# Optimization experiments

Measured on AMD Instinct MI355X. Metric: run time of the kernel, lower is better.

Reference implementation:

```python
import jax, jax.numpy as jnp
import numpy as np

V, E, H, B, T = 50000, 300, 512, 256, 64
D_OUT = 3
EPS = 1e-5


def setup_inputs() -> dict:
    key = jax.random.key(0)
    ks = jax.random.split(key, 16)
    s = lambda k, shape: (jax.random.normal(k, shape, jnp.float32) * 0.05)
    return {
        "premise": jax.random.randint(ks[0], (T, B), 0, V),
        "hypothesis": jax.random.randint(ks[1], (T, B), 0, V),
        "embed": s(ks[2], (V, E)),
        "W_ih": s(ks[3], (4 * H, E)),
        "W_hh": s(ks[4], (4 * H, H)),
        "b_ih": s(ks[5], (4 * H,)),
        "b_hh": s(ks[6], (4 * H,)),
        "bn0_g": jnp.ones((4 * H,), jnp.float32),
        "bn0_b": jnp.zeros((4 * H,), jnp.float32),
        "W0": s(ks[7], (4 * H, 4 * H)),
        "b0": s(ks[8], (4 * H,)),
        "bn1_g": jnp.ones((4 * H,), jnp.float32),
        "bn1_b": jnp.zeros((4 * H,), jnp.float32),
        "W1": s(ks[9], (4 * H, 4 * H)),
        "b1": s(ks[10], (4 * H,)),
        "bno_g": jnp.ones((4 * H,), jnp.float32),
        "bno_b": jnp.zeros((4 * H,), jnp.float32),
        "Wo": s(ks[11], (D_OUT, 4 * H)),
        "bo": s(ks[12], (D_OUT,)),
    }


def _lstm_final_h(xs, W_ih, W_hh, bias):
    # xs: [T, N, E]; shared-weight LSTMCell scan, returns final hidden [N, H]
    x_proj = jnp.einsum('tne,ge->tng', xs, W_ih) + bias  # hoist input GEMM out of the recurrence
    n = xs.shape[1]
    h0 = jnp.zeros((n, H), xs.dtype)

    def step(carry, xg):
        h, c = carry
        gates = xg + h @ W_hh.T
        i, f, g, o = jnp.split(gates, 4, axis=-1)  # torch LSTMCell gate order
        c = jax.nn.sigmoid(f) * c + jax.nn.sigmoid(i) * jnp.tanh(g)
        h = jax.nn.sigmoid(o) * jnp.tanh(c)
        return (h, c), None

    (h, _), _ = jax.lax.scan(step, (h0, h0), x_proj)
    return h


def _bn(x, g, b):
    # BatchNorm1d in training mode: biased batch stats
    mu = x.mean(0)
    var = x.var(0)
    return (x - mu) * jax.lax.rsqrt(var + EPS) * g + b


def reference(premise, hypothesis, embed, W_ih, W_hh, b_ih, b_hh,
              bn0_g, bn0_b, W0, b0, bn1_g, bn1_b, W1, b1,
              bno_g, bno_b, Wo, bo):
    p = embed[premise]      # [T, B, E]
    hyp = embed[hypothesis]  # [T, B, E]
    combined = jnp.concatenate([p, hyp], axis=1)  # [T, 2B, E]
    bias = b_ih + b_hh
    h_fw = _lstm_final_h(combined, W_ih, W_hh, bias)          # forward direction
    h_bw = _lstm_final_h(combined[::-1], W_ih, W_hh, bias)    # backward direction (shared cell)
    feat = jnp.concatenate([h_fw[:B], h_bw[:B], h_fw[B:], h_bw[B:]], axis=1)  # [B, 4H]
    x = jax.nn.relu(_bn(feat, bn0_g, bn0_b) @ W0.T + b0)
    x = jax.nn.relu(_bn(x, bn1_g, bn1_b) @ W1.T + b1)
    return _bn(x, bno_g, bno_b) @ Wo.T + bo  # [B, d_out]
```

## Files before the change

kernel.cpp:

```cpp
#include <hip/hip_runtime.h>
#include <hip/hip_bf16.h>


typedef __attribute__((ext_vector_type(8))) short bf16x8;
typedef __attribute__((ext_vector_type(4))) float f32x4;
typedef __attribute__((ext_vector_type(2))) unsigned int u32x2;

#define DEVI __device__ __forceinline__

template<int N> struct IC { static constexpr int v = N; };

template<int AUX> DEVI void async16t(const void* g, void* l) {
  __builtin_amdgcn_global_load_lds((const __attribute__((address_space(1))) void*)g,
                                   (__attribute__((address_space(3))) void*)l,
                                   16, 0, AUX);
}
DEVI void async16(const void* g, void* l) { async16t<0>(g, l); }
DEVI u32x2 load8_pin(const void* addr) {
  u32x2 r;
  asm volatile("global_load_dwordx2 %0, %1, off" : "=v"(r) : "v"(addr) : "memory");
  return r;
}
DEVI void storeh_coh(void* a, unsigned int v) {
  asm volatile("global_store_short %0, %1, off sc0 sc1" ::"v"(a), "v"(v) : "memory");
}
template<int N> DEVI void vmwait_barrier() {
  asm volatile("s_waitcnt vmcnt(%0)" ::"i"(N) : "memory");
  __builtin_amdgcn_s_barrier();
  __builtin_amdgcn_sched_barrier(0);
}
DEVI float sigmf_(float x) { return 1.f / (1.f + __expf(-x)); }
DEVI float tanhf_(float x) {
  float a = __expf(-2.f * fabsf(x));
  float t = (1.f - a) / (1.f + a);
  return copysignf(t, x);
}
DEVI __hip_bfloat16 f2b(float x) { return __float2bfloat16(x); }
DEVI float b2f(__hip_bfloat16 x) { return __bfloat162float(x); }

__global__ void cvt_f32_bf16(const float* __restrict__ src,
                             __hip_bfloat16* __restrict__ dst, int n4) {
  int i = blockIdx.x * 256 + threadIdx.x;
  int stride = gridDim.x * 256;
  for (; i < n4; i += stride) {
    float4 v = ((const float4*)src)[i];
    union { __hip_bfloat16 h[4]; uint2 u; } o;
    o.h[0] = f2b(v.x); o.h[1] = f2b(v.y); o.h[2] = f2b(v.z); o.h[3] = f2b(v.w);
    ((uint2*)dst)[i] = o.u;
  }
}

__global__ void pack_wih(const float* __restrict__ W_ih,
                         const float* __restrict__ b_ih,
                         const float* __restrict__ b_hh,
                         __hip_bfloat16* __restrict__ WihP,
                         float* __restrict__ biasL) {
  int tid = blockIdx.x * 256 + threadIdx.x;
  int stride = gridDim.x * 256;
  for (int i = tid; i < 2048 * 320; i += stride) {
    int r = i / 320, c = i - r * 320;
    WihP[i] = (c < 300) ? f2b(W_ih[r * 300 + c]) : f2b(0.f);
  }
  if (tid < 2048) biasL[tid] = b_ih[tid] + b_hh[tid];
}

__global__ void gather_kernel(const int* __restrict__ prem, const int* __restrict__ hyp,
                              const float* __restrict__ embed,
                              __hip_bfloat16* __restrict__ Ain) {
  int row = blockIdx.x * 4 + (threadIdx.x >> 6);
  int lane = threadIdx.x & 63;
  int tt = row >> 9, n = row & 511;
  int tok = (n < 256) ? prem[tt * 256 + n] : hyp[tt * 256 + (n - 256)];
  const float4* e4 = (const float4*)(embed + (size_t)tok * 300);
  uint2* d2 = (uint2*)(Ain + (size_t)row * 320);
  for (int j = lane; j < 75; j += 64) {
    float4 v = e4[j];
    union { __hip_bfloat16 h[4]; uint2 u; } o;
    o.h[0] = f2b(v.x); o.h[1] = f2b(v.y); o.h[2] = f2b(v.z); o.h[3] = f2b(v.w);
    d2[j] = o.u;
  }
  for (int j = 75 + lane; j < 80; j += 64) d2[j] = make_uint2(0u, 0u);
}

template<int BM, int EPI>
__global__ __launch_bounds__(256)
void gemm_pipe(const __hip_bfloat16* __restrict__ A,
               const __hip_bfloat16* __restrict__ Bn,
               const float* __restrict__ bias,
               void* __restrict__ Cout, int K, int ldc) {
  constexpr int BK = 64;
  constexpr int ABYT = BM * BK * 2;
  constexpr int BBYT = 128 * BK * 2;
  constexpr int APW = BM / 32;
  constexpr int IFL = APW + 4;
  constexpr int WM = BM / 2, MT = WM / 16;
  __shared__ alignas(16) char smem[2 * ABYT + 2 * BBYT];

  const int tid = threadIdx.x, lane = tid & 63, wid = tid >> 6;
  const int wrow = wid >> 1, wcol = wid & 1;
  const int m0 = blockIdx.x * BM, n0 = blockIdx.y * 128;
  const int l8 = lane & 7, ld8 = lane >> 3;
  const int swz = (l8 ^ ld8) * 8;

  const __hip_bfloat16* Abase = A + (size_t)m0 * K;
  const __hip_bfloat16* Bbase = Bn + (size_t)n0 * K;

  f32x4 acc[MT][4];
#pragma unroll
  for (int i = 0; i < MT; ++i)
#pragma unroll
    for (int j = 0; j < 4; ++j) acc[i][j] = {0.f, 0.f, 0.f, 0.f};

  auto stage = [&](int buf, int kt) {
    const __hip_bfloat16* as = Abase + kt * BK + swz;
    char* ad = smem + buf * ABYT;
#pragma unroll
    for (int s = 0; s < APW; ++s) {
      int iss = wid * APW + s;
      async16(as + (size_t)(iss * 8 + ld8) * K, ad + iss * 1024);
    }
    const __hip_bfloat16* bs = Bbase + kt * BK + swz;
    char* bd = smem + 2 * ABYT + buf * BBYT;
#pragma unroll
    for (int s = 0; s < 4; ++s) {
      int iss = wid * 4 + s;
      async16(bs + (size_t)(iss * 8 + ld8) * K, bd + iss * 1024);
    }
  };

  const int nk = K / BK;
  stage(0, 0);
  for (int kt = 0; kt < nk; ++kt) {
    if (kt + 1 < nk) {
      stage((kt + 1) & 1, kt + 1);
      vmwait_barrier<IFL>();
    } else {
      vmwait_barrier<0>();
    }
    const __hip_bfloat16* ab = (const __hip_bfloat16*)(smem + (kt & 1) * ABYT);
    const __hip_bfloat16* bb = (const __hip_bfloat16*)(smem + 2 * ABYT + (kt & 1) * BBYT);
#pragma unroll
    for (int kk = 0; kk < BK; kk += 32) {
      bf16x8 af[MT], bf[4];
#pragma unroll
      for (int i = 0; i < MT; ++i) {
        int r = wrow * WM + i * 16 + (lane & 15);
        af[i] = *(const bf16x8*)&ab[r * BK + ((kk + (lane >> 4) * 8) ^ ((r & 7) * 8))];
      }
#pragma unroll
      for (int j = 0; j < 4; ++j) {
        int r = wcol * 64 + j * 16 + (lane & 15);
        bf[j] = *(const bf16x8*)&bb[r * BK + ((kk + (lane >> 4) * 8) ^ ((r & 7) * 8))];
      }
#pragma unroll
      for (int i = 0; i < MT; ++i)
#pragma unroll
        for (int j = 0; j < 4; ++j)
          acc[i][j] = __builtin_amdgcn_mfma_f32_16x16x32_bf16(af[i], bf[j], acc[i][j], 0, 0, 0);
    }
    __builtin_amdgcn_s_barrier();
  }

  if (EPI == 2) {
#pragma unroll
    for (int i = 0; i < MT; ++i)
#pragma unroll
      for (int j = 0; j < 4; ++j) {
        union { __hip_bfloat16 h[4]; uint2 u; } o;
#pragma unroll
        for (int rr = 0; rr < 4; ++rr) o.h[rr] = f2b(acc[i][j][rr]);
        size_t slot = (((size_t)blockIdx.x * 16 + blockIdx.y) * 4 + wid) * 16 + i * 4 + j;
        *(uint2*)((char*)Cout + slot * 512 + lane * 8) = o.u;
      }
    return;
  }

  __syncthreads();
  float* Csm = (float*)smem;
#pragma unroll
  for (int i = 0; i < MT; ++i)
#pragma unroll
    for (int j = 0; j < 4; ++j)
#pragma unroll
      for (int rr = 0; rr < 4; ++rr) {
        int row = wrow * WM + i * 16 + (lane >> 4) * 4 + rr;
        int col = wcol * 64 + j * 16 + (lane & 15);
        Csm[row * 128 + (col ^ ((row & 7) << 2))] = acc[i][j][rr];
      }
  __syncthreads();
#pragma unroll
  for (int it = 0; it < BM / 16; ++it) {
    int idx = it * 256 + tid;
    int row = idx >> 4;
    int cb = (idx & 15) * 8;
    int sw = (row & 7) << 2;
    float4 v0 = *(const float4*)&Csm[row * 128 + (cb ^ sw)];
    float4 v1 = *(const float4*)&Csm[row * 128 + ((cb + 4) ^ sw)];
    float4 b0 = *(const float4*)&bias[n0 + cb];
    float4 b1 = *(const float4*)&bias[n0 + cb + 4];
    v0.x = fmaxf(v0.x + b0.x, 0.f); v0.y = fmaxf(v0.y + b0.y, 0.f);
    v0.z = fmaxf(v0.z + b0.z, 0.f); v0.w = fmaxf(v0.w + b0.w, 0.f);
    v1.x = fmaxf(v1.x + b1.x, 0.f); v1.y = fmaxf(v1.y + b1.y, 0.f);
    v1.z = fmaxf(v1.z + b1.z, 0.f); v1.w = fmaxf(v1.w + b1.w, 0.f);
    size_t base = (size_t)(m0 + row) * ldc + n0 + cb;
    *(float4*)&((float*)Cout)[base] = v0;
    *(float4*)&((float*)Cout)[base + 4] = v1;
  }
}

__global__ __launch_bounds__(256, 2)
void lstm_persist(const __hip_bfloat16* __restrict__ xp,
                  const __hip_bfloat16* __restrict__ Whh,
                  const float* __restrict__ biasL,
                  __hip_bfloat16* __restrict__ hA,
                  __hip_bfloat16* __restrict__ hB,
                  int* __restrict__ ctr) {
  extern __shared__ char smem[];
  const int tid = threadIdx.x, lane = tid & 63, wid = tid >> 6;
  const int bid = blockIdx.x;
  const int grp = (bid & 7) | ((bid >> 8) << 3);
  const int jt2 = (bid >> 3) & 31;
  const int m0 = grp * 64;
  const int l8 = lane & 7, ld8 = lane >> 3;
  const int swz = (l8 ^ ld8) * 8;

  bf16x8 w[16];
  for (int hh = 0; hh < 2; ++hh) {
#pragma unroll
    for (int kt2 = 0; kt2 < 4; ++kt2)
#pragma unroll
      for (int s = 0; s < 2; ++s) {
        int iss = wid * 2 + s;
        int r = iss * 8 + ld8;
        int Wrow = (r >> 4) * 512 + jt2 * 16 + (r & 15);
        async16(Whh + (size_t)Wrow * 512 + (hh * 4 + kt2) * 64 + swz,
                smem + kt2 * 8192 + iss * 1024);
      }
    asm volatile("s_waitcnt vmcnt(0)" ::: "memory");
    __builtin_amdgcn_s_barrier();
    __builtin_amdgcn_sched_barrier(0);
    {
      const __hip_bfloat16* wb = (const __hip_bfloat16*)smem;
      int r = wid * 16 + (lane & 15);
#pragma unroll
      for (int kt2 = 0; kt2 < 4; ++kt2)
#pragma unroll
        for (int kkh = 0; kkh < 2; ++kkh)
          w[(hh * 4 + kt2) * 2 + kkh] =
              *(const bf16x8*)&wb[kt2 * 4096 + r * 64 +
                                  ((kkh * 32 + (lane >> 4) * 8) ^ ((r & 7) * 8))];
    }
    __syncthreads();
  }

  int* flag = (int*)(smem + 49152);
  if (tid == 0) {
    int xcd = (int)(__builtin_amdgcn_s_getreg((31 << 11) | 20) & 15);
    int o1 = atomicOr(&ctr[grp * 64 + 1], 1 << xcd);
    int o2 = atomicOr(&ctr[1025], 1 << xcd);
    asm volatile("" ::"v"(o1), "v"(o2));
    atomicAdd(&ctr[1024], 1);
    while (__hip_atomic_load(&ctr[1024], __ATOMIC_RELAXED, __HIP_MEMORY_SCOPE_AGENT) < 512)
      __builtin_amdgcn_s_sleep(2);
    int gm = __hip_atomic_load(&ctr[grp * 64 + 1], __ATOMIC_RELAXED, __HIP_MEMORY_SCOPE_AGENT);
    int am = __hip_atomic_load(&ctr[1025], __ATOMIC_RELAXED, __HIP_MEMORY_SCOPE_AGENT);
    *flag = (__popc((unsigned)gm) == 1 && __popc((unsigned)am) == 8) ? 1 : 0;
  }
  __syncthreads();
  const bool fastpath = (*flag != 0);
  __syncthreads();

  const int q = lane >> 4, c = lane & 15;
  const int widx = (grp & 1) * 2 + ((jt2 & 7) >> 2);
  const int jx = jt2 & 3;
  const int byb = jt2 >> 3;
  float bias_[4];
#pragma unroll
  for (int g = 0; g < 4; ++g) bias_[g] = biasL[g * 512 + jt2 * 16 + c];

  float c_[4];
#pragma unroll
  for (int e = 0; e < 4; ++e) c_[e] = 0.f;

  auto run = [&](auto FC) {
    constexpr bool FAST = decltype(FC)::v;
    constexpr int AUX = FAST ? 1 : 17;
    for (int t = 0; t < 64; ++t) {
      const __hip_bfloat16* hin = (t & 1) ? hB : hA;
      __hip_bfloat16* hout = (t & 1) ? hA : hB;

      auto issueA = [&](int kt) {
#pragma unroll
        for (int s = 0; s < 2; ++s) {
          int iss = wid * 2 + s;
          async16t<AUX>(hin + (size_t)(m0 + iss * 8 + ld8) * 512 + kt * 64 + swz,
                        smem + (kt & 3) * 8192 + iss * 1024);
        }
      };
      issueA(0); issueA(1); issueA(2);
      __builtin_amdgcn_sched_barrier(0);
      const int xbase = (grp < 8) ? (t * 512 + m0) : ((63 - t) * 512 + (m0 - 512));
      const int bx = xbase >> 7;
      u32x2 xg[4];
#pragma unroll
      for (int g = 0; g < 4; ++g) {
        size_t slot = (((size_t)bx * 16 + g * 4 + byb) * 4 + widx) * 16 + wid * 4 + jx;
        xg[g] = load8_pin((const char*)xp + slot * 512 + lane * 8);
      }
      __builtin_amdgcn_sched_barrier(0);

      f32x4 acc[4];
#pragma unroll
      for (int i = 0; i < 4; ++i) acc[i] = {0.f, 0.f, 0.f, 0.f};

      auto do_kt = [&](auto K) {
        constexpr int KT = decltype(K)::v;
        constexpr int WT[8] = {8, 8, 8, 4, 4, 4, 2, 0};
        vmwait_barrier<WT[KT]>();
        if constexpr (KT < 5) issueA(KT + 3);
        const __hip_bfloat16* ab = (const __hip_bfloat16*)(smem + (KT & 3) * 8192);
#pragma unroll
        for (int kk = 0; kk < 64; kk += 32) {
          bf16x8 af[4];
#pragma unroll
          for (int i = 0; i < 4; ++i) {
            int r = i * 16 + (lane & 15);
            af[i] = *(const bf16x8*)&ab[r * 64 + ((kk + (lane >> 4) * 8) ^ ((r & 7) * 8))];
          }
#pragma unroll
          for (int i = 0; i < 4; ++i)
            acc[i] = __builtin_amdgcn_mfma_f32_16x16x32_bf16(
                af[i], w[KT * 2 + kk / 32], acc[i], 0, 0, 0);
        }
      };
      do_kt(IC<0>{}); do_kt(IC<1>{}); do_kt(IC<2>{}); do_kt(IC<3>{});
      do_kt(IC<4>{}); do_kt(IC<5>{}); do_kt(IC<6>{}); do_kt(IC<7>{});

      float* gsm = (float*)(smem + 32768);
#pragma unroll
      for (int i = 0; i < 4; ++i)
        *(f32x4*)(gsm + (wid * 4 + i) * 256 + lane * 4) = acc[i];
      __syncthreads();
      f32x4 gq[4];
#pragma unroll
      for (int g = 0; g < 4; ++g)
        gq[g] = *(const f32x4*)(gsm + (g * 4 + wid) * 256 + lane * 4);
      asm volatile("s_waitcnt vmcnt(0)" ::: "memory");
      __builtin_amdgcn_sched_barrier(0);

      union { u32x2 v; __hip_bfloat16 h[4]; } X[4];
#pragma unroll
      for (int g = 0; g < 4; ++g) X[g].v = xg[g];
      __hip_bfloat16* hbase = hout + (size_t)(m0 + wid * 16 + q * 4) * 512 + jt2 * 16 + c;
#pragma unroll
      for (int rr = 0; rr < 4; ++rr) {
        float gi = gq[0][rr] + b2f(X[0].h[rr]) + bias_[0];
        float gf = gq[1][rr] + b2f(X[1].h[rr]) + bias_[1];
        float gg = gq[2][rr] + b2f(X[2].h[rr]) + bias_[2];
        float go = gq[3][rr] + b2f(X[3].h[rr]) + bias_[3];
        float cn = sigmf_(gf) * c_[rr] + sigmf_(gi) * tanhf_(gg);
        float hn = sigmf_(go) * tanhf_(cn);
        c_[rr] = cn;
        union { __hip_bfloat16 b; unsigned short u; } hb;
        hb.b = f2b(hn);
        if constexpr (FAST) {
          hbase[rr * 512] = hb.b;
        } else {
          storeh_coh(hbase + rr * 512, (unsigned int)hb.u);
        }
      }
      asm volatile("s_waitcnt vmcnt(0)" ::: "memory");
      __syncthreads();

      if (t < 63) {
        if (tid == 0) {
          const int target = 32 * (t + 1);
          int got = atomicAdd(&ctr[grp * 64], 1) + 1;
          if (got < target) {
            while (__hip_atomic_load(&ctr[grp * 64], __ATOMIC_RELAXED,
                                     __HIP_MEMORY_SCOPE_AGENT) < target)
              __builtin_amdgcn_s_sleep(1);
          }
        }
        __syncthreads();
      }
    }
  };
  if (fastpath) run(IC<1>{});
  else          run(IC<0>{});
}

__global__ void feat_kernel(const __hip_bfloat16* __restrict__ hA, float* __restrict__ feat) {
  int b = blockIdx.x;
  for (int c = threadIdx.x; c < 2048; c += 256) {
    int sec = c >> 9, j = c & 511;
    int row = (sec == 0) ? b : (sec == 1) ? 512 + b : (sec == 2) ? 256 + b : 768 + b;
    feat[b * 2048 + c] = b2f(hA[(size_t)row * 512 + j]);
  }
}

__global__ void bn_stats(const float* __restrict__ x, const float* __restrict__ g,
                         const float* __restrict__ b,
                         float* __restrict__ sc, float* __restrict__ sh) {
  int c = blockIdx.x * 256 + threadIdx.x;
  float s = 0.f, s2 = 0.f;
  for (int r = 0; r < 256; ++r) {
    float v = x[r * 2048 + c];
    s += v;
    s2 += v * v;
  }
  float mu = s * (1.f / 256.f);
  float var = s2 * (1.f / 256.f) - mu * mu;
  float rs = rsqrtf(var + 1e-5f);
  float scale = g[c] * rs;
  sc[c] = scale;
  sh[c] = b[c] - mu * scale;
}

__global__ void bn_apply(const float* __restrict__ x, const float* __restrict__ sc,
                         const float* __restrict__ sh, __hip_bfloat16* __restrict__ xn) {
  int i = blockIdx.x * 256 + threadIdx.x;
  int c = i & 2047;
  xn[i] = f2b(x[i] * sc[c] + sh[c]);
}

__global__ void final_kernel(const float* __restrict__ x2, const float* __restrict__ sc,
                             const float* __restrict__ sh, const float* __restrict__ Wo,
                             const float* __restrict__ bo, float* __restrict__ out) {
  __shared__ float red[3][256];
  int b = blockIdx.x, tid = threadIdx.x;
  float a0 = 0.f, a1 = 0.f, a2 = 0.f;
  for (int c = tid; c < 2048; c += 256) {
    float v = x2[b * 2048 + c] * sc[c] + sh[c];
    a0 += v * Wo[c];
    a1 += v * Wo[2048 + c];
    a2 += v * Wo[4096 + c];
  }
  red[0][tid] = a0; red[1][tid] = a1; red[2][tid] = a2;
  __syncthreads();
  for (int s = 128; s > 0; s >>= 1) {
    if (tid < s) {
      red[0][tid] += red[0][tid + s];
      red[1][tid] += red[1][tid + s];
      red[2][tid] += red[2][tid + s];
    }
    __syncthreads();
  }
  if (tid < 3) out[b * 3 + tid] = red[tid][0] + bo[tid];
}

extern "C" void kernel_launch(void* const* d_in, const int* in_sizes, int n_in,
                              void* d_out, int out_size, void* d_ws, size_t ws_size,
                              hipStream_t stream) {
  (void)in_sizes; (void)n_in; (void)out_size; (void)ws_size;
  const int* prem = (const int*)d_in[0];
  const int* hyp = (const int*)d_in[1];
  const float* embed = (const float*)d_in[2];
  const float* W_ih = (const float*)d_in[3];
  const float* W_hh = (const float*)d_in[4];
  const float* b_ih = (const float*)d_in[5];
  const float* b_hh = (const float*)d_in[6];
  const float* bn0g = (const float*)d_in[7];
  const float* bn0b = (const float*)d_in[8];
  const float* W0 = (const float*)d_in[9];
  const float* b0 = (const float*)d_in[10];
  const float* bn1g = (const float*)d_in[11];
  const float* bn1b = (const float*)d_in[12];
  const float* W1 = (const float*)d_in[13];
  const float* b1 = (const float*)d_in[14];
  const float* bnog = (const float*)d_in[15];
  const float* bnob = (const float*)d_in[16];
  const float* Wo = (const float*)d_in[17];
  const float* bo = (const float*)d_in[18];
  float* out = (float*)d_out;

  char* w = (char*)d_ws;
  size_t off = 0;
  auto alloc = [&](size_t bytes) {
    void* p = w + off;
    off += (bytes + 255) & ~(size_t)255;
    return p;
  };
  __hip_bfloat16* WihP = (__hip_bfloat16*)alloc((size_t)2048 * 320 * 2);
  __hip_bfloat16* Whhb = (__hip_bfloat16*)alloc((size_t)2048 * 512 * 2);
  __hip_bfloat16* W0b = (__hip_bfloat16*)alloc((size_t)2048 * 2048 * 2);
  __hip_bfloat16* W1b = (__hip_bfloat16*)alloc((size_t)2048 * 2048 * 2);
  float* biasL = (float*)alloc(2048 * 4);
  int* ctr = (int*)alloc(2048 * 4);
  __hip_bfloat16* xp = (__hip_bfloat16*)alloc((size_t)32768 * 2048 * 2);
  size_t ain_off = off;
  __hip_bfloat16* Ain = (__hip_bfloat16*)alloc((size_t)32768 * 320 * 2);
  size_t end_off = off;
  off = ain_off;
  __hip_bfloat16* hA = (__hip_bfloat16*)alloc((size_t)1024 * 512 * 2);
  __hip_bfloat16* hB = (__hip_bfloat16*)alloc((size_t)1024 * 512 * 2);
  float* feat = (float*)alloc((size_t)256 * 2048 * 4);
  __hip_bfloat16* xn = (__hip_bfloat16*)alloc((size_t)256 * 2048 * 2);
  float* x1 = (float*)alloc((size_t)256 * 2048 * 4);
  float* x2 = (float*)alloc((size_t)256 * 2048 * 4);
  float* sc0 = (float*)alloc(2048 * 4);
  float* sh0 = (float*)alloc(2048 * 4);
  float* sc1 = (float*)alloc(2048 * 4);
  float* sh1 = (float*)alloc(2048 * 4);
  float* sc2 = (float*)alloc(2048 * 4);
  float* sh2 = (float*)alloc(2048 * 4);
  (void)end_off;

  (void)hipMemsetAsync(ctr, 0, 2048 * 4, stream);
  pack_wih<<<512, 256, 0, stream>>>(W_ih, b_ih, b_hh, WihP, biasL);
  cvt_f32_bf16<<<1024, 256, 0, stream>>>(W_hh, Whhb, 2048 * 512 / 4);
  cvt_f32_bf16<<<2048, 256, 0, stream>>>(W0, W0b, 2048 * 2048 / 4);
  cvt_f32_bf16<<<2048, 256, 0, stream>>>(W1, W1b, 2048 * 2048 / 4);
  gather_kernel<<<8192, 256, 0, stream>>>(prem, hyp, embed, Ain);
  gemm_pipe<128, 2><<<dim3(256, 16), 256, 0, stream>>>(Ain, WihP, biasL, xp, 320, 2048);
  (void)hipMemsetAsync(hA, 0, (size_t)1024 * 512 * 2, stream);
  (void)hipFuncSetAttribute(reinterpret_cast<const void*>(lstm_persist),
                            hipFuncAttributeMaxDynamicSharedMemorySize, 65536);
  lstm_persist<<<512, 256, 49408, stream>>>(xp, Whhb, biasL, hA, hB, ctr);
  feat_kernel<<<256, 256, 0, stream>>>(hA, feat);
  bn_stats<<<8, 256, 0, stream>>>(feat, bn0g, bn0b, sc0, sh0);
  bn_apply<<<2048, 256, 0, stream>>>(feat, sc0, sh0, xn);
  gemm_pipe<64, 1><<<dim3(4, 16), 256, 0, stream>>>(xn, W0b, b0, x1, 2048, 2048);
  bn_stats<<<8, 256, 0, stream>>>(x1, bn1g, bn1b, sc1, sh1);
  bn_apply<<<2048, 256, 0, stream>>>(x1, sc1, sh1, xn);
  gemm_pipe<64, 1><<<dim3(4, 16), 256, 0, stream>>>(xn, W1b, b1, x2, 2048, 2048);
  bn_stats<<<8, 256, 0, stream>>>(x2, bnog, bnob, sc2, sh2);
  final_kernel<<<256, 256, 0, stream>>>(x2, sc2, sh2, Wo, bo, out);
}
```

Measured before the change: 471.6 us.

## Retile persistent LSTM to 32-row groups with per-tile step flags

Changes the persistent LSTM tiling from 64-row groups with 16 hidden columns per block to 32-row groups with 32 hidden columns per block. Each block now reads half as many h rows per step and keeps a 2x16 weight fragment set in registers. The per-group atomic-add counter barrier is replaced by per-tile step flags: each block stores its completed step and waits only until all 16 tiles of its group have reached it. This aims to shrink the h traffic per step and the cost of the cross-block barrier in the recurrence, at the cost of more weight registers and more flag polling.

```diff
diff --git a/kernel.cpp b/kernel.cpp
--- a/kernel.cpp
+++ b/kernel.cpp
@@ -218,65 +218,68 @@
   extern __shared__ char smem[];
   const int tid = threadIdx.x, lane = tid & 63, wid = tid >> 6;
   const int bid = blockIdx.x;
-  const int grp = (bid & 7) | ((bid >> 8) << 3);
-  const int jt2 = (bid >> 3) & 31;
-  const int m0 = grp * 64;
+  const int gi = (bid & 7) | ((bid >> 7) << 3);
+  const int jt = (bid >> 3) & 15;
+  const int gl = (gi < 16) ? gi : gi - 16;
+  const int m0 = (gi < 16) ? gi * 32 : 512 + gl * 32;
   const int l8 = lane & 7, ld8 = lane >> 3;
   const int swz = (l8 ^ ld8) * 8;
 
-  bf16x8 w[16];
-  for (int hh = 0; hh < 2; ++hh) {
-#pragma unroll
-    for (int kt2 = 0; kt2 < 4; ++kt2)
-#pragma unroll
-      for (int s = 0; s < 2; ++s) {
-        int iss = wid * 2 + s;
-        int r = iss * 8 + ld8;
-        int Wrow = (r >> 4) * 512 + jt2 * 16 + (r & 15);
-        async16(Whh + (size_t)Wrow * 512 + (hh * 4 + kt2) * 64 + swz,
-                smem + kt2 * 8192 + iss * 1024);
-      }
+  bf16x8 w[2][16];
+#pragma unroll
+  for (int kt = 0; kt < 8; ++kt) {
+#pragma unroll
+    for (int s = 0; s < 4; ++s) {
+      int lr32 = s * 8 + ld8;
+      int Wrow = wid * 512 + jt * 32 + lr32;
+      async16(Whh + (size_t)Wrow * 512 + kt * 64 + swz,
+              smem + wid * 4096 + s * 1024);
+    }
     asm volatile("s_waitcnt vmcnt(0)" ::: "memory");
     __builtin_amdgcn_s_barrier();
     __builtin_amdgcn_sched_barrier(0);
     {
-      const __hip_bfloat16* wb = (const __hip_bfloat16*)smem;
-      int r = wid * 16 + (lane & 15);
-#pragma unroll
-      for (int kt2 = 0; kt2 < 4; ++kt2)
+      const __hip_bfloat16* wb = (const __hip_bfloat16*)(smem + wid * 4096);
+#pragma unroll
+      for (int j = 0; j < 2; ++j) {
+        int r = j * 16 + (lane & 15);
 #pragma unroll
         for (int kkh = 0; kkh < 2; ++kkh)
-          w[(hh * 4 + kt2) * 2 + kkh] =
-              *(const bf16x8*)&wb[kt2 * 4096 + r * 64 +
-                                  ((kkh * 32 + (lane >> 4) * 8) ^ ((r & 7) * 8))];
+          w[j][kt * 2 + kkh] =
+              *(const bf16x8*)&wb[r * 64 + ((kkh * 32 + (lane >> 4) * 8) ^ ((r & 7) * 8))];
+      }
     }
     __syncthreads();
   }
 
-  int* flag = (int*)(smem + 49152);
+  int* flag = (int*)(smem + 32768);
   if (tid == 0) {
     int xcd = (int)(__builtin_amdgcn_s_getreg((31 << 11) | 20) & 15);
-    int o1 = atomicOr(&ctr[grp * 64 + 1], 1 << xcd);
-    int o2 = atomicOr(&ctr[1025], 1 << xcd);
+    int o1 = atomicOr(&ctr[512 + gi], 1 << xcd);
+    int o2 = atomicOr(&ctr[561], 1 << xcd);
     asm volatile("" ::"v"(o1), "v"(o2));
-    atomicAdd(&ctr[1024], 1);
-    while (__hip_atomic_load(&ctr[1024], __ATOMIC_RELAXED, __HIP_MEMORY_SCOPE_AGENT) < 512)
+    atomicAdd(&ctr[560], 1);
+    while (__hip_atomic_load(&ctr[560], __ATOMIC_RELAXED, __HIP_MEMORY_SCOPE_AGENT) < 512)
       __builtin_amdgcn_s_sleep(2);
-    int gm = __hip_atomic_load(&ctr[grp * 64 + 1], __ATOMIC_RELAXED, __HIP_MEMORY_SCOPE_AGENT);
-    int am = __hip_atomic_load(&ctr[1025], __ATOMIC_RELAXED, __HIP_MEMORY_SCOPE_AGENT);
+    int gm = __hip_atomic_load(&ctr[512 + gi], __ATOMIC_RELAXED, __HIP_MEMORY_SCOPE_AGENT);
+    int am = __hip_atomic_load(&ctr[561], __ATOMIC_RELAXED, __HIP_MEMORY_SCOPE_AGENT);
     *flag = (__popc((unsigned)gm) == 1 && __popc((unsigned)am) == 8) ? 1 : 0;
   }
   __syncthreads();
   const bool fastpath = (*flag != 0);
   __syncthreads();
 
-  const int q = lane >> 4, c = lane & 15;
-  const int widx = (grp & 1) * 2 + ((jt2 & 7) >> 2);
-  const int jx = jt2 & 3;
-  const int byb = jt2 >> 3;
+  const int rq = tid >> 5;
+  const int col = tid & 31;
+  const int i_x = (gl & 1) * 2 + (rq >> 2);
+  const int wid_x = ((gl & 3) >> 1) * 2 + ((jt & 3) >> 1);
+  const int j_x = (jt & 1) * 2 + (col >> 4);
+  const int lane_x = ((rq & 3) << 4) | (col & 15);
+  const int lprime = ((rq & 3) << 4) | (col & 15);
+
   float bias_[4];
 #pragma unroll
-  for (int g = 0; g < 4; ++g) bias_[g] = biasL[g * 512 + jt2 * 16 + c];
+  for (int g = 0; g < 4; ++g) bias_[g] = biasL[g * 512 + jt * 32 + col];
 
   float c_[4];
 #pragma unroll
@@ -289,76 +292,96 @@
       const __hip_bfloat16* hin = (t & 1) ? hB : hA;
       __hip_bfloat16* hout = (t & 1) ? hA : hB;
 
+      if (t > 0) {
+        if (wid == 0) {
+          bool ok;
+          do {
+            int v = __hip_atomic_load(&ctr[gi * 16 + (lane & 15)], __ATOMIC_RELAXED,
+                                      __HIP_MEMORY_SCOPE_AGENT);
+            ok = __all(v >= t);
+            if (!ok) __builtin_amdgcn_s_sleep(1);
+          } while (!ok);
+        }
+        __syncthreads();
+      }
+
+      const int TT = (gi < 16) ? t : 63 - t;
+      const int bx = TT * 4 + (gl >> 2);
+      u32x2 xg[4];
+#pragma unroll
+      for (int g = 0; g < 4; ++g) {
+        int by = g * 4 + (jt >> 2);
+        size_t slot = (((size_t)bx * 16 + by) * 4 + wid_x) * 16 + i_x * 4 + j_x;
+        xg[g] = load8_pin((const char*)xp + slot * 512 + lane_x * 8);
+      }
+      __builtin_amdgcn_sched_barrier(0);
+
       auto issueA = [&](int kt) {
-#pragma unroll
-        for (int s = 0; s < 2; ++s) {
-          int iss = wid * 2 + s;
-          async16t<AUX>(hin + (size_t)(m0 + iss * 8 + ld8) * 512 + kt * 64 + swz,
-                        smem + (kt & 3) * 8192 + iss * 1024);
-        }
+        async16t<AUX>(hin + (size_t)(m0 + wid * 8 + ld8) * 512 + kt * 64 + swz,
+                      smem + (kt & 3) * 4096 + wid * 1024);
       };
       issueA(0); issueA(1); issueA(2);
       __builtin_amdgcn_sched_barrier(0);
-      const int xbase = (grp < 8) ? (t * 512 + m0) : ((63 - t) * 512 + (m0 - 512));
-      const int bx = xbase >> 7;
-      u32x2 xg[4];
-#pragma unroll
-      for (int g = 0; g < 4; ++g) {
-        size_t slot = (((size_t)bx * 16 + g * 4 + byb) * 4 + widx) * 16 + wid * 4 + jx;
-        xg[g] = load8_pin((const char*)xp + slot * 512 + lane * 8);
-      }
-      __builtin_amdgcn_sched_barrier(0);
-
-      f32x4 acc[4];
-#pragma unroll
-      for (int i = 0; i < 4; ++i) acc[i] = {0.f, 0.f, 0.f, 0.f};
+
+      f32x4 acc[2][2];
+#pragma unroll
+      for (int i = 0; i < 2; ++i)
+#pragma unroll
+        for (int j = 0; j < 2; ++j) acc[i][j] = {0.f, 0.f, 0.f, 0.f};
 
       auto do_kt = [&](auto K) {
         constexpr int KT = decltype(K)::v;
-        constexpr int WT[8] = {8, 8, 8, 4, 4, 4, 2, 0};
+        constexpr int WT[8] = {2, 2, 2, 2, 2, 2, 1, 0};
         vmwait_barrier<WT[KT]>();
         if constexpr (KT < 5) issueA(KT + 3);
-        const __hip_bfloat16* ab = (const __hip_bfloat16*)(smem + (KT & 3) * 8192);
+        const __hip_bfloat16* ab = (const __hip_bfloat16*)(smem + (KT & 3) * 4096);
 #pragma unroll
         for (int kk = 0; kk < 64; kk += 32) {
-          bf16x8 af[4];
-#pragma unroll
-          for (int i = 0; i < 4; ++i) {
+          bf16x8 af[2];
+#pragma unroll
+          for (int i = 0; i < 2; ++i) {
             int r = i * 16 + (lane & 15);
             af[i] = *(const bf16x8*)&ab[r * 64 + ((kk + (lane >> 4) * 8) ^ ((r & 7) * 8))];
           }
 #pragma unroll
-          for (int i = 0; i < 4; ++i)
-            acc[i] = __builtin_amdgcn_mfma_f32_16x16x32_bf16(
-                af[i], w[KT * 2 + kk / 32], acc[i], 0, 0, 0);
+          for (int i = 0; i < 2; ++i)
+#pragma unroll
+            for (int j = 0; j < 2; ++j)
+              acc[i][j] = __builtin_amdgcn_mfma_f32_16x16x32_bf16(
+                  af[i], w[j][KT * 2 + kk / 32], acc[i][j], 0, 0, 0);
         }
       };
       do_kt(IC<0>{}); do_kt(IC<1>{}); do_kt(IC<2>{}); do_kt(IC<3>{});
       do_kt(IC<4>{}); do_kt(IC<5>{}); do_kt(IC<6>{}); do_kt(IC<7>{});
 
-      float* gsm = (float*)(smem + 32768);
-#pragma unroll
-      for (int i = 0; i < 4; ++i)
-        *(f32x4*)(gsm + (wid * 4 + i) * 256 + lane * 4) = acc[i];
+      float* gsm = (float*)(smem + 16384);
+#pragma unroll
+      for (int i = 0; i < 2; ++i)
+#pragma unroll
+        for (int j = 0; j < 2; ++j)
+          *(f32x4*)(gsm + (wid * 4 + i * 2 + j) * 256 + lane * 4) = acc[i][j];
       __syncthreads();
       f32x4 gq[4];
-#pragma unroll
-      for (int g = 0; g < 4; ++g)
-        gq[g] = *(const f32x4*)(gsm + (g * 4 + wid) * 256 + lane * 4);
+      {
+        const int iq = rq >> 2, jq = col >> 4;
+#pragma unroll
+        for (int g = 0; g < 4; ++g)
+          gq[g] = *(const f32x4*)(gsm + (g * 4 + iq * 2 + jq) * 256 + lprime * 4);
+      }
       asm volatile("s_waitcnt vmcnt(0)" ::: "memory");
       __builtin_amdgcn_sched_barrier(0);
 
       union { u32x2 v; __hip_bfloat16 h[4]; } X[4];
 #pragma unroll
       for (int g = 0; g < 4; ++g) X[g].v = xg[g];
-      __hip_bfloat16* hbase = hout + (size_t)(m0 + wid * 16 + q * 4) * 512 + jt2 * 16 + c;
+      __hip_bfloat16* hbase = hout + (size_t)(m0 + rq * 4) * 512 + jt * 32 + col;
 #pragma unroll
       for (int rr = 0; rr < 4; ++rr) {
-        float gi = gq[0][rr] + b2f(X[0].h[rr]) + bias_[0];
+        float gi_ = gq[0][rr] + b2f(X[0].h[rr]) + bias_[0];
         float gf = gq[1][rr] + b2f(X[1].h[rr]) + bias_[1];
         float gg = gq[2][rr] + b2f(X[2].h[rr]) + bias_[2];
         float go = gq[3][rr] + b2f(X[3].h[rr]) + bias_[3];
-        float cn = sigmf_(gf) * c_[rr] + sigmf_(gi) * tanhf_(gg);
+        float cn = sigmf_(gf) * c_[rr] + sigmf_(gi_) * tanhf_(gg);
         float hn = sigmf_(go) * tanhf_(cn);
         c_[rr] = cn;
         union { __hip_bfloat16 b; unsigned short u; } hb;
@@ -371,19 +394,9 @@
       }
       asm volatile("s_waitcnt vmcnt(0)" ::: "memory");
       __syncthreads();
-
-      if (t < 63) {
-        if (tid == 0) {
-          const int target = 32 * (t + 1);
-          int got = atomicAdd(&ctr[grp * 64], 1) + 1;
-          if (got < target) {
-            while (__hip_atomic_load(&ctr[grp * 64], __ATOMIC_RELAXED,
-                                     __HIP_MEMORY_SCOPE_AGENT) < target)
-              __builtin_amdgcn_s_sleep(1);
-          }
-        }
-        __syncthreads();
-      }
+      if (tid == 0)
+        __hip_atomic_store(&ctr[gi * 16 + jt], t + 1, __ATOMIC_RELAXED,
+                           __HIP_MEMORY_SCOPE_AGENT);
     }
   };
   if (fastpath) run(IC<1>{});
@@ -486,7 +499,7 @@
   __hip_bfloat16* W0b = (__hip_bfloat16*)alloc((size_t)2048 * 2048 * 2);
   __hip_bfloat16* W1b = (__hip_bfloat16*)alloc((size_t)2048 * 2048 * 2);
   float* biasL = (float*)alloc(2048 * 4);
-  int* ctr = (int*)alloc(2048 * 4);
+  int* ctr = (int*)alloc(1024 * 4);
   __hip_bfloat16* xp = (__hip_bfloat16*)alloc((size_t)32768 * 2048 * 2);
   size_t ain_off = off;
   __hip_bfloat16* Ain = (__hip_bfloat16*)alloc((size_t)32768 * 320 * 2);
@@ -506,7 +519,7 @@
   float* sh2 = (float*)alloc(2048 * 4);
   (void)end_off;
 
-  (void)hipMemsetAsync(ctr, 0, 2048 * 4, stream);
+  (void)hipMemsetAsync(ctr, 0, 1024 * 4, stream);
   pack_wih<<<512, 256, 0, stream>>>(W_ih, b_ih, b_hh, WihP, biasL);
   cvt_f32_bf16<<<1024, 256, 0, stream>>>(W_hh, Whhb, 2048 * 512 / 4);
   cvt_f32_bf16<<<2048, 256, 0, stream>>>(W0, W0b, 2048 * 2048 / 4);
@@ -516,7 +529,7 @@
   (void)hipMemsetAsync(hA, 0, (size_t)1024 * 512 * 2, stream);
   (void)hipFuncSetAttribute(reinterpret_cast<const void*>(lstm_persist),
                             hipFuncAttributeMaxDynamicSharedMemorySize, 65536);
-  lstm_persist<<<512, 256, 49408, stream>>>(xp, Whhb, biasL, hA, hB, ctr);
+  lstm_persist<<<512, 256, 33024, stream>>>(xp, Whhb, biasL, hA, hB, ctr);
   feat_kernel<<<256, 256, 0, stream>>>(hA, feat);
   bn_stats<<<8, 256, 0, stream>>>(feat, bn0g, bn0b, sc0, sh0);
   bn_apply<<<2048, 256, 0, stream>>>(feat, sc0, sh0, xn);
```

After: 455.2 us. 3.5% less time.
